# Kernel tuning notes

Hardware: AMD Instinct MI355X
Metric: run time of the kernel (lower is better)

The kernel has to match this reference:

```python
import jax, jax.numpy as jnp
import numpy as np

WINDOW_SIZE = 7
NB_HEADS = 8


def _relative_position_index(ws: int) -> np.ndarray:
    coords = np.stack(np.meshgrid(np.arange(ws), np.arange(ws), indexing='ij'))  # [2, ws, ws]
    flat = coords.reshape(2, -1)  # [2, ws*ws]
    rel = flat[:, :, None] - flat[:, None, :]  # [2, N, N]
    rel = rel.transpose(1, 2, 0)
    rel[:, :, 0] += ws - 1
    rel[:, :, 1] += ws - 1
    rel[:, :, 0] *= 2 * ws - 1
    return rel.sum(-1).astype(np.int64)  # [N, N]


def setup_inputs() -> dict:
    key = jax.random.key(0)
    ks = jax.random.split(key, 7)
    B_, N, C = 2048, WINDOW_SIZE * WINDOW_SIZE, 256
    nW = 64
    return {
        'x': jax.random.normal(ks[0], (B_, N, C), dtype=jnp.float32),
        'mask': jax.random.normal(ks[1], (nW, N, N), dtype=jnp.float32),
        'qkv_w': jax.random.normal(ks[2], (C, 3 * C), dtype=jnp.float32) * 0.02,
        'qkv_b': jax.random.normal(ks[3], (3 * C,), dtype=jnp.float32) * 0.02,
        'proj_w': jax.random.normal(ks[4], (C, C), dtype=jnp.float32) * 0.02,
        'proj_b': jax.random.normal(ks[5], (C,), dtype=jnp.float32) * 0.02,
        'bias_table': jax.random.normal(ks[6], ((2 * WINDOW_SIZE - 1) ** 2, NB_HEADS), dtype=jnp.float32) * 0.02,
    }


def reference(x, mask, qkv_w, qkv_b, proj_w, proj_b, bias_table):
    B_, N, C = x.shape
    h = NB_HEADS
    d = C // h
    rpi = jnp.asarray(_relative_position_index(WINDOW_SIZE))  # [N, N] int

    qkv = x @ qkv_w + qkv_b  # [B_, N, 3C]
    qkv = qkv.reshape(B_, N, 3, h, d).transpose(2, 0, 3, 1, 4)  # [3, B_, h, N, d]
    q, k, v = qkv[0], qkv[1], qkv[2]

    scale = d ** -0.5
    attn = jnp.einsum('bhnd,bhmd->bhnm', q * scale, k)  # [B_, h, N, N]

    # relative position bias gather: [N*N, h] -> [h, N, N]
    bias = bias_table[rpi.reshape(-1)].reshape(N, N, h).transpose(2, 0, 1)
    attn = attn + bias[None]

    nW = mask.shape[0]
    attn = attn.reshape(B_ // nW, nW, h, N, N) + mask[None, :, None]  # broadcast mask over heads
    attn = attn.reshape(B_, h, N, N)
    attn = jax.nn.softmax(attn, axis=-1)

    out = jnp.einsum('bhnm,bhmd->bhnd', attn, v)  # [B_, h, N, d]
    out = out.transpose(0, 2, 1, 3).reshape(B_, N, C)
    return out @ proj_w + proj_b
```

## Files before the change

### kernel.cpp

```cpp
#include <hip/hip_runtime.h>
#include <hip/hip_bf16.h>

typedef __attribute__((ext_vector_type(8))) short bf16x8;
typedef __attribute__((ext_vector_type(4))) float f32x4;

__device__ __forceinline__ void load_lds16(const void* g, void* l) {
    __builtin_amdgcn_global_load_lds(
        (const __attribute__((address_space(1))) unsigned int*)g,
        (__attribute__((address_space(3))) unsigned int*)l, 16, 0, 0);
}

__global__ void k_cvt_x(const float* __restrict__ x, __hip_bfloat16* __restrict__ xb, int n4) {
    for (int i = blockIdx.x * blockDim.x + threadIdx.x; i < n4; i += gridDim.x * blockDim.x) {
        float4 v = ((const float4*)x)[i];
        union { ushort4 u; __hip_bfloat16 h[4]; } o;
        o.h[0] = __float2bfloat16(v.x); o.h[1] = __float2bfloat16(v.y);
        o.h[2] = __float2bfloat16(v.z); o.h[3] = __float2bfloat16(v.w);
        ((ushort4*)xb)[i] = o.u;
    }
}

__global__ void k_prep(const float* __restrict__ qkv_w, const float* __restrict__ qkv_b,
                       const float* __restrict__ proj_w, const float* __restrict__ bias_table,
                       const float* __restrict__ mask,
                       __hip_bfloat16* __restrict__ qwT, __hip_bfloat16* __restrict__ pwT,
                       float* __restrict__ qb_s, float* __restrict__ cbt) {
    const float scale = 0.17677669529663687f;
    const int P1 = 768 * 256, P2 = P1 + 256 * 256, P3 = P2 + 768, P4 = P3 + 64 * 8 * 4 * 4 * 64;
    int i = blockIdx.x * 256 + threadIdx.x;
    if (i < P1) {
        int nc = i >> 8, kc = i & 255;
        float v = qkv_w[kc * 768 + nc];
        if (nc < 256) v *= scale;
        qwT[i] = __float2bfloat16(v);
    } else if (i < P2) {
        int j = i - P1;
        int nc = j >> 8, kc = j & 255;
        pwT[j] = __float2bfloat16(proj_w[kc * 256 + nc]);
    } else if (i < P3) {
        int j = i - P2;
        qb_s[j] = qkv_b[j] * (j < 256 ? scale : 1.f);
    } else if (i < P4) {
        int j = i - P3;
        int w = j >> 13;
        int h = (j >> 10) & 7;
        int rt = (j >> 8) & 3;
        int ct = (j >> 6) & 3;
        int lane = j & 63;
        int m = ct * 16 + (lane & 15);
        f32x4 v;
#pragma unroll
        for (int reg = 0; reg < 4; ++reg) {
            int n = rt * 16 + 4 * (lane >> 4) + reg;
            float val;
            if (m >= 49) val = -1e30f;
            else if (n >= 49) val = 0.f;
            else {
                int i1 = n / 7, j1 = n % 7, i2 = m / 7, j2 = m % 7;
                int rpi = (i1 - i2 + 6) * 13 + (j1 - j2 + 6);
                val = bias_table[rpi * 8 + h] + mask[(w * 49 + n) * 49 + m];
            }
            v[reg] = val;
        }
        ((f32x4*)cbt)[j] = v;
    }
}

template <bool OUT_BF16>
__global__ __launch_bounds__(256, 2)
void gemm_bt(const __hip_bfloat16* __restrict__ A,
             const __hip_bfloat16* __restrict__ BT,
             const float* __restrict__ bias,
             void* __restrict__ Cout,
             int M, int N, int K, int gridN) {
    __shared__ alignas(16) __hip_bfloat16 sA[2][128][64];
    __shared__ alignas(16) __hip_bfloat16 sB[2][128][64];
    const int nwg = gridDim.x, bid = blockIdx.x;
    const int qq = nwg >> 3, rr = nwg & 7;
    const int xc = bid & 7, oo = bid >> 3;
    const int wg = (xc < rr ? xc * (qq + 1) : rr * (qq + 1) + (xc - rr) * qq) + oo;
    const int bm = wg / gridN, bn = wg % gridN;

    const int tid = threadIdx.x, wid = tid >> 6, lane = tid & 63;
    const int g = lane >> 4, c0 = lane & 15;
    const int r8 = lane >> 3;
    const int sl = (lane & 7) ^ r8;
    const int wrow = (wid >> 1) * 64, wcol = (wid & 1) * 64;
    const __hip_bfloat16* Abase = A + (size_t)bm * 128 * K;
    const __hip_bfloat16* Bbase = BT + (size_t)bn * 128 * K;
    const int KT = K >> 6;

    f32x4 acc[4][4];
#pragma unroll
    for (int i = 0; i < 4; ++i)
#pragma unroll
        for (int j = 0; j < 4; ++j)
#pragma unroll
            for (int r = 0; r < 4; ++r) acc[i][j][r] = 0.f;

    auto stage = [&](int buf, int kt) {
        const __hip_bfloat16* Ak = Abase + kt * 64;
        const __hip_bfloat16* Bk = Bbase + kt * 64;
        char* la = (char*)&sA[buf][0][0];
        char* lb = (char*)&sB[buf][0][0];
#pragma unroll
        for (int i = 0; i < 4; ++i) {
            int chunk = wid * 4 + i;
            int row = chunk * 8 + r8;
            load_lds16(Ak + (size_t)row * K + sl * 8, la + chunk * 1024);
            load_lds16(Bk + (size_t)row * K + sl * 8, lb + chunk * 1024);
        }
    };

    stage(0, 0);
    __syncthreads();
    for (int kt = 0; kt < KT; ++kt) {
        int cur = kt & 1;
        if (kt + 1 < KT) stage(cur ^ 1, kt + 1);
        const char* la = (const char*)&sA[cur][0][0];
        const char* lb = (const char*)&sB[cur][0][0];
#pragma unroll
        for (int ks = 0; ks < 2; ++ks) {
            bf16x8 af[4], bfr[4];
            int sbyte = ((ks * 4 + g) ^ (c0 & 7)) * 16;
#pragma unroll
            for (int t = 0; t < 4; ++t) {
                int ra = wrow + t * 16 + c0;
                af[t] = *(const bf16x8*)(la + ra * 128 + sbyte);
                int rb = wcol + t * 16 + c0;
                bfr[t] = *(const bf16x8*)(lb + rb * 128 + sbyte);
            }
#pragma unroll
            for (int rt = 0; rt < 4; ++rt)
#pragma unroll
                for (int ct = 0; ct < 4; ++ct)
                    acc[rt][ct] = __builtin_amdgcn_mfma_f32_16x16x32_bf16(
                        af[rt], bfr[ct], acc[rt][ct], 0, 0, 0);
        }
        __syncthreads();
    }

    float bv[4];
#pragma unroll
    for (int ct = 0; ct < 4; ++ct) bv[ct] = bias[bn * 128 + wcol + ct * 16 + c0];
#pragma unroll
    for (int rt = 0; rt < 4; ++rt) {
#pragma unroll
        for (int ct = 0; ct < 4; ++ct) {
#pragma unroll
            for (int reg = 0; reg < 4; ++reg) {
                int row = bm * 128 + wrow + rt * 16 + g * 4 + reg;
                int col = bn * 128 + wcol + ct * 16 + c0;
                float v = acc[rt][ct][reg] + bv[ct];
                if (OUT_BF16)
                    ((__hip_bfloat16*)Cout)[(size_t)row * N + col] = __float2bfloat16(v);
                else
                    ((float*)Cout)[(size_t)row * N + col] = v;
            }
        }
    }
}

__global__ __launch_bounds__(64)
void attn_win(const __hip_bfloat16* __restrict__ qkv,
              const float* __restrict__ cbt,
              __hip_bfloat16* __restrict__ attout) {
    __shared__ alignas(16) __hip_bfloat16 vt[32][72];
    __shared__ alignas(16) __hip_bfloat16 pl[52][64];
    const int blk = blockIdx.x;
    const int w = blk >> 8, h = (blk >> 5) & 7, rep = blk & 31;
    const int b = rep * 64 + w;
    const int lane = threadIdx.x & 63, g = lane >> 4, c0 = lane & 15;
    const __hip_bfloat16* qb = qkv + (size_t)b * 49 * 768 + h * 32;
    const bf16x8 z8 = {};

    bf16x8 kf[4], qf[4];
#pragma unroll
    for (int ct = 0; ct < 4; ++ct) {
        int m = ct * 16 + c0;
        kf[ct] = (m < 49) ? *(const bf16x8*)(qb + (size_t)m * 768 + 256 + g * 8) : z8;
    }
#pragma unroll
    for (int rt = 0; rt < 4; ++rt) {
        int n = rt * 16 + c0;
        qf[rt] = (n < 49) ? *(const bf16x8*)(qb + (size_t)n * 768 + g * 8) : z8;
    }

#pragma unroll
    for (int it = 0; it < 4; ++it) {
        int q = it * 64 + lane;
        int m = q >> 2, c8 = (q & 3) * 8;
        if (m < 49) {
            bf16x8 v8 = *(const bf16x8*)(qb + (size_t)m * 768 + 512 + c8);
#pragma unroll
            for (int j = 0; j < 8; ++j)
                *(short*)&vt[c8 + j][m] = v8[j];
        }
    }
    for (int i = lane; i < 32 * 15; i += 64) {
        int c = i / 15, m = 49 + i % 15;
        vt[c][m] = __float2bfloat16(0.f);
    }

    const f32x4* cbb = (const f32x4*)cbt + ((size_t)(w * 8 + h)) * 1024;
    const f32x4 zf = {0.f, 0.f, 0.f, 0.f};

#pragma unroll
    for (int rt = 0; rt < 4; ++rt) {
        f32x4 cb[4];
#pragma unroll
        for (int ct = 0; ct < 4; ++ct) cb[ct] = cbb[(rt * 4 + ct) * 64 + lane];
        f32x4 s[4];
        __builtin_amdgcn_s_setprio(1);
#pragma unroll
        for (int ct = 0; ct < 4; ++ct)
            s[ct] = __builtin_amdgcn_mfma_f32_16x16x32_bf16(qf[rt], kf[ct], zf, 0, 0, 0);
        __builtin_amdgcn_s_setprio(0);
#pragma unroll
        for (int ct = 0; ct < 4; ++ct)
#pragma unroll
            for (int reg = 0; reg < 4; ++reg) s[ct][reg] += cb[ct][reg];
#pragma unroll
        for (int reg = 0; reg < 4; ++reg) {
            int n = rt * 16 + 4 * g + reg;
            float mx = fmaxf(fmaxf(s[0][reg], s[1][reg]), fmaxf(s[2][reg], s[3][reg]));
            mx = fmaxf(mx, __shfl_xor(mx, 1));
            mx = fmaxf(mx, __shfl_xor(mx, 2));
            mx = fmaxf(mx, __shfl_xor(mx, 4));
            mx = fmaxf(mx, __shfl_xor(mx, 8));
            float sum = 0.f;
#pragma unroll
            for (int ct = 0; ct < 4; ++ct) {
                float e = __expf(s[ct][reg] - mx);
                s[ct][reg] = e;
                sum += e;
            }
            sum += __shfl_xor(sum, 1);
            sum += __shfl_xor(sum, 2);
            sum += __shfl_xor(sum, 4);
            sum += __shfl_xor(sum, 8);
            float inv = 1.f / sum;
            if (n < 52) {
#pragma unroll
                for (int ct = 0; ct < 4; ++ct) {
                    int m = ct * 16 + c0;
                    int byte = (n * 128 + m * 2) ^ ((n & 7) << 4);
                    *(__hip_bfloat16*)((char*)&pl[0][0] + byte) = __float2bfloat16(s[ct][reg] * inv);
                }
            }
        }
    }
    __syncthreads();

    f32x4 o[4][2];
#pragma unroll
    for (int rt = 0; rt < 4; ++rt)
#pragma unroll
        for (int ci = 0; ci < 2; ++ci)
#pragma unroll
            for (int r = 0; r < 4; ++r) o[rt][ci][r] = 0.f;
#pragma unroll
    for (int kt = 0; kt < 2; ++kt) {
        bf16x8 pa[4], vb[2];
#pragma unroll
        for (int rt = 0; rt < 4; ++rt) {
            int row = rt * 16 + c0;
            int rc = row < 52 ? row : 51;
            int byte = rc * 128 + (((kt * 4 + g) ^ (rc & 7)) << 4);
            pa[rt] = *(const bf16x8*)((const char*)&pl[0][0] + byte);
        }
#pragma unroll
        for (int ci = 0; ci < 2; ++ci)
            vb[ci] = *(const bf16x8*)(&vt[ci * 16 + c0][kt * 32 + g * 8]);
        __builtin_amdgcn_s_setprio(1);
#pragma unroll
        for (int rt = 0; rt < 4; ++rt)
#pragma unroll
            for (int ci = 0; ci < 2; ++ci)
                o[rt][ci] = __builtin_amdgcn_mfma_f32_16x16x32_bf16(pa[rt], vb[ci], o[rt][ci], 0, 0, 0);
        __builtin_amdgcn_s_setprio(0);
    }
    __hip_bfloat16* ob = attout + (size_t)b * 49 * 256 + h * 32;
#pragma unroll
    for (int rt = 0; rt < 4; ++rt) {
#pragma unroll
        for (int reg = 0; reg < 4; ++reg) {
            int n = rt * 16 + 4 * g + reg;
            if (n < 49) {
#pragma unroll
                for (int ci = 0; ci < 2; ++ci)
                    ob[(size_t)n * 256 + ci * 16 + c0] = __float2bfloat16(o[rt][ci][reg]);
            }
        }
    }
}

extern "C" void kernel_launch(void* const* d_in, const int* in_sizes, int n_in,
                              void* d_out, int out_size, void* d_ws, size_t ws_size,
                              hipStream_t stream) {
    const float* x          = (const float*)d_in[0];
    const float* mask       = (const float*)d_in[1];
    const float* qkv_w      = (const float*)d_in[2];
    const float* qkv_b      = (const float*)d_in[3];
    const float* proj_w     = (const float*)d_in[4];
    const float* proj_b     = (const float*)d_in[5];
    const float* bias_table = (const float*)d_in[6];

    const int C = 256, N3 = 768, NN = 49;
    const int M  = in_sizes[0] / C;
    const int B_ = M / NN;

    char* ws = (char*)d_ws;
    __hip_bfloat16* qkv_ws = (__hip_bfloat16*)ws;
    size_t off = (size_t)M * N3 * 2;
    __hip_bfloat16* xb  = (__hip_bfloat16*)(ws + off);
    __hip_bfloat16* att = xb;
    off += (size_t)M * C * 2;
    __hip_bfloat16* qwT = (__hip_bfloat16*)(ws + off); off += (size_t)N3 * C * 2;
    __hip_bfloat16* pwT = (__hip_bfloat16*)(ws + off); off += (size_t)C * C * 2;
    float* qb_s = (float*)(ws + off); off += (size_t)N3 * 4;
    float* cbt  = (float*)(ws + off); off += (size_t)64 * 8 * 4096 * 4;

    int n4 = (int)((size_t)M * C / 4);
    k_cvt_x<<<2048, 256, 0, stream>>>(x, xb, n4);
    int prep_total = 768 * 256 + 256 * 256 + 768 + 64 * 8 * 4 * 4 * 64;
    k_prep<<<(prep_total + 255) / 256, 256, 0, stream>>>(qkv_w, qkv_b, proj_w, bias_table, mask,
                                                         qwT, pwT, qb_s, cbt);
    gemm_bt<true><<<(N3 / 128) * (M / 128), 256, 0, stream>>>(xb, qwT, qb_s, qkv_ws, M, N3, C, N3 / 128);
    attn_win<<<B_ * 8, 64, 0, stream>>>(qkv_ws, cbt, att);
    gemm_bt<false><<<(C / 128) * (M / 128), 256, 0, stream>>>(att, pwT, proj_b, d_out, M, C, C, C / 128);
}
```

Baseline: 362.7 us.

## Fuse x conversion, QKV GEMM, window attention and projection into one kernel

Replaces the separate x-to-bf16 conversion, tiled QKV GEMM, per-head attention kernel and projection GEMM with a single kernel that handles one window per 512-thread block, with one wave per head. The window's x, Q/K/V, softmax probabilities and attention output stay in LDS, so the bf16 copy of x and the qkv and attention intermediates are never written to or read back from HBM. In exchange, every block re-reads the full QKV and projection weight matrices from global memory (expected to be served mostly from L2) with no LDS staging. The roughly 148 KB of LDS per block also limits occupancy to very few waves per CU.

After: 371.4 us. 2.4% more time.

```diff
diff --git a/kernel.cpp b/kernel.cpp
--- a/kernel.cpp
+++ b/kernel.cpp
@@ -4,20 +4,9 @@
 typedef __attribute__((ext_vector_type(8))) short bf16x8;
 typedef __attribute__((ext_vector_type(4))) float f32x4;
 
-__device__ __forceinline__ void load_lds16(const void* g, void* l) {
-    __builtin_amdgcn_global_load_lds(
-        (const __attribute__((address_space(1))) unsigned int*)g,
-        (__attribute__((address_space(3))) unsigned int*)l, 16, 0, 0);
-}
-
-__global__ void k_cvt_x(const float* __restrict__ x, __hip_bfloat16* __restrict__ xb, int n4) {
-    for (int i = blockIdx.x * blockDim.x + threadIdx.x; i < n4; i += gridDim.x * blockDim.x) {
-        float4 v = ((const float4*)x)[i];
-        union { ushort4 u; __hip_bfloat16 h[4]; } o;
-        o.h[0] = __float2bfloat16(v.x); o.h[1] = __float2bfloat16(v.y);
-        o.h[2] = __float2bfloat16(v.z); o.h[3] = __float2bfloat16(v.w);
-        ((ushort4*)xb)[i] = o.u;
-    }
+static __device__ __forceinline__ short b16(float f) {
+    __hip_bfloat16 h = __float2bfloat16(f);
+    return *reinterpret_cast<short*>(&h);
 }
 
 __global__ void k_prep(const float* __restrict__ qkv_w, const float* __restrict__ qkv_b,
@@ -66,143 +55,104 @@
     }
 }
 
-template <bool OUT_BF16>
-__global__ __launch_bounds__(256, 2)
-void gemm_bt(const __hip_bfloat16* __restrict__ A,
-             const __hip_bfloat16* __restrict__ BT,
-             const float* __restrict__ bias,
-             void* __restrict__ Cout,
-             int M, int N, int K, int gridN) {
-    __shared__ alignas(16) __hip_bfloat16 sA[2][128][64];
-    __shared__ alignas(16) __hip_bfloat16 sB[2][128][64];
-    const int nwg = gridDim.x, bid = blockIdx.x;
-    const int qq = nwg >> 3, rr = nwg & 7;
-    const int xc = bid & 7, oo = bid >> 3;
-    const int wg = (xc < rr ? xc * (qq + 1) : rr * (qq + 1) + (xc - rr) * qq) + oo;
-    const int bm = wg / gridN, bn = wg % gridN;
-
-    const int tid = threadIdx.x, wid = tid >> 6, lane = tid & 63;
-    const int g = lane >> 4, c0 = lane & 15;
-    const int r8 = lane >> 3;
-    const int sl = (lane & 7) ^ r8;
-    const int wrow = (wid >> 1) * 64, wcol = (wid & 1) * 64;
-    const __hip_bfloat16* Abase = A + (size_t)bm * 128 * K;
-    const __hip_bfloat16* Bbase = BT + (size_t)bn * 128 * K;
-    const int KT = K >> 6;
-
-    f32x4 acc[4][4];
-#pragma unroll
-    for (int i = 0; i < 4; ++i)
-#pragma unroll
-        for (int j = 0; j < 4; ++j)
-#pragma unroll
-            for (int r = 0; r < 4; ++r) acc[i][j][r] = 0.f;
-
-    auto stage = [&](int buf, int kt) {
-        const __hip_bfloat16* Ak = Abase + kt * 64;
-        const __hip_bfloat16* Bk = Bbase + kt * 64;
-        char* la = (char*)&sA[buf][0][0];
-        char* lb = (char*)&sB[buf][0][0];
-#pragma unroll
-        for (int i = 0; i < 4; ++i) {
-            int chunk = wid * 4 + i;
-            int row = chunk * 8 + r8;
-            load_lds16(Ak + (size_t)row * K + sl * 8, la + chunk * 1024);
-            load_lds16(Bk + (size_t)row * K + sl * 8, lb + chunk * 1024);
-        }
-    };
-
-    stage(0, 0);
+#define XS_OFF    0
+#define PL_OFF(h) ((h) * 6272)
+#define QK_OFF    50176
+#define QS(h)     (QK_OFF + (h) * 8000)
+#define KS(h)     (QK_OFF + (h) * 8000 + 4000)
+#define AS_OFF    QK_OFF
+#define VT(h)     (114176 + (h) * 4608)
+#define LDS_TOTAL 151040
+
+__global__ __launch_bounds__(512, 2)
+void win_fused(const float* __restrict__ x,
+               const __hip_bfloat16* __restrict__ qwT,
+               const __hip_bfloat16* __restrict__ pwT,
+               const float* __restrict__ qb_s,
+               const float* __restrict__ proj_b,
+               const float* __restrict__ cbt,
+               float* __restrict__ out) {
+    __shared__ alignas(16) char lds[LDS_TOTAL];
+    const int b = blockIdx.x;
+    const int tid = threadIdx.x;
+    const int h = tid >> 6, lane = tid & 63, g = lane >> 4, c0 = lane & 15;
+
+    const float* xw = x + (size_t)b * 12544;
+    for (int i = tid; i < 3136; i += 512) {
+        int row = i >> 6, col4 = i & 63;
+        float4 v = *(const float4*)(xw + row * 256 + col4 * 4);
+        union { unsigned long long u; short s[4]; } o;
+        o.s[0] = b16(v.x); o.s[1] = b16(v.y); o.s[2] = b16(v.z); o.s[3] = b16(v.w);
+        int byte = row * 512 + (((col4 >> 1) ^ (row & 7)) << 4) + (col4 & 1) * 8;
+        *(unsigned long long*)(lds + byte) = o.u;
+    }
     __syncthreads();
-    for (int kt = 0; kt < KT; ++kt) {
-        int cur = kt & 1;
-        if (kt + 1 < KT) stage(cur ^ 1, kt + 1);
-        const char* la = (const char*)&sA[cur][0][0];
-        const char* lb = (const char*)&sB[cur][0][0];
-#pragma unroll
-        for (int ks = 0; ks < 2; ++ks) {
-            bf16x8 af[4], bfr[4];
-            int sbyte = ((ks * 4 + g) ^ (c0 & 7)) * 16;
-#pragma unroll
-            for (int t = 0; t < 4; ++t) {
-                int ra = wrow + t * 16 + c0;
-                af[t] = *(const bf16x8*)(la + ra * 128 + sbyte);
-                int rb = wcol + t * 16 + c0;
-                bfr[t] = *(const bf16x8*)(lb + rb * 128 + sbyte);
-            }
-#pragma unroll
-            for (int rt = 0; rt < 4; ++rt)
-#pragma unroll
-                for (int ct = 0; ct < 4; ++ct)
-                    acc[rt][ct] = __builtin_amdgcn_mfma_f32_16x16x32_bf16(
-                        af[rt], bfr[ct], acc[rt][ct], 0, 0, 0);
-        }
-        __syncthreads();
-    }
-
-    float bv[4];
-#pragma unroll
-    for (int ct = 0; ct < 4; ++ct) bv[ct] = bias[bn * 128 + wcol + ct * 16 + c0];
-#pragma unroll
-    for (int rt = 0; rt < 4; ++rt) {
-#pragma unroll
-        for (int ct = 0; ct < 4; ++ct) {
-#pragma unroll
-            for (int reg = 0; reg < 4; ++reg) {
-                int row = bm * 128 + wrow + rt * 16 + g * 4 + reg;
-                int col = bn * 128 + wcol + ct * 16 + c0;
-                float v = acc[rt][ct][reg] + bv[ct];
-                if (OUT_BF16)
-                    ((__hip_bfloat16*)Cout)[(size_t)row * N + col] = __float2bfloat16(v);
-                else
-                    ((float*)Cout)[(size_t)row * N + col] = v;
-            }
-        }
-    }
-}
-
-__global__ __launch_bounds__(64)
-void attn_win(const __hip_bfloat16* __restrict__ qkv,
-              const float* __restrict__ cbt,
-              __hip_bfloat16* __restrict__ attout) {
-    __shared__ alignas(16) __hip_bfloat16 vt[32][72];
-    __shared__ alignas(16) __hip_bfloat16 pl[52][64];
-    const int blk = blockIdx.x;
-    const int w = blk >> 8, h = (blk >> 5) & 7, rep = blk & 31;
-    const int b = rep * 64 + w;
-    const int lane = threadIdx.x & 63, g = lane >> 4, c0 = lane & 15;
-    const __hip_bfloat16* qb = qkv + (size_t)b * 49 * 768 + h * 32;
-    const bf16x8 z8 = {};
-
-    bf16x8 kf[4], qf[4];
-#pragma unroll
-    for (int ct = 0; ct < 4; ++ct) {
-        int m = ct * 16 + c0;
-        kf[ct] = (m < 49) ? *(const bf16x8*)(qb + (size_t)m * 768 + 256 + g * 8) : z8;
-    }
-#pragma unroll
-    for (int rt = 0; rt < 4; ++rt) {
-        int n = rt * 16 + c0;
-        qf[rt] = (n < 49) ? *(const bf16x8*)(qb + (size_t)n * 768 + g * 8) : z8;
-    }
-
-#pragma unroll
-    for (int it = 0; it < 4; ++it) {
-        int q = it * 64 + lane;
-        int m = q >> 2, c8 = (q & 3) * 8;
-        if (m < 49) {
-            bf16x8 v8 = *(const bf16x8*)(qb + (size_t)m * 768 + 512 + c8);
-#pragma unroll
-            for (int j = 0; j < 8; ++j)
-                *(short*)&vt[c8 + j][m] = v8[j];
-        }
-    }
-    for (int i = lane; i < 32 * 15; i += 64) {
-        int c = i / 15, m = 49 + i % 15;
-        vt[c][m] = __float2bfloat16(0.f);
-    }
-
-    const f32x4* cbb = (const f32x4*)cbt + ((size_t)(w * 8 + h)) * 1024;
+
+    f32x4 acc[3][4][2];
+#pragma unroll
+    for (int q3 = 0; q3 < 3; ++q3)
+#pragma unroll
+        for (int rt = 0; rt < 4; ++rt)
+#pragma unroll
+            for (int ct2 = 0; ct2 < 2; ++ct2)
+#pragma unroll
+                for (int r = 0; r < 4; ++r) acc[q3][rt][ct2][r] = 0.f;
+
+#pragma unroll
+    for (int kt = 0; kt < 8; ++kt) {
+        bf16x8 af[4];
+#pragma unroll
+        for (int rt = 0; rt < 4; ++rt) {
+            int row = rt * 16 + c0;
+            af[rt] = *(const bf16x8*)(lds + row * 512 + (((kt * 4 + g) ^ (c0 & 7)) << 4));
+        }
+#pragma unroll
+        for (int q3 = 0; q3 < 3; ++q3) {
+#pragma unroll
+            for (int ct2 = 0; ct2 < 2; ++ct2) {
+                bf16x8 bw = *(const bf16x8*)(qwT + (size_t)(q3 * 256 + h * 32 + ct2 * 16 + c0) * 256
+                                             + kt * 32 + g * 8);
+#pragma unroll
+                for (int rt = 0; rt < 4; ++rt)
+                    acc[q3][rt][ct2] = __builtin_amdgcn_mfma_f32_16x16x32_bf16(
+                        af[rt], bw, acc[q3][rt][ct2], 0, 0, 0);
+            }
+        }
+    }
+#pragma unroll
+    for (int q3 = 0; q3 < 3; ++q3) {
+#pragma unroll
+        for (int ct2 = 0; ct2 < 2; ++ct2) {
+            float bias = qb_s[q3 * 256 + h * 32 + ct2 * 16 + c0];
+            int d0 = ct2 * 16 + c0;
+#pragma unroll
+            for (int rt = 0; rt < 4; ++rt) {
+#pragma unroll
+                for (int reg = 0; reg < 4; ++reg) {
+                    int n = rt * 16 + 4 * g + reg;
+                    if (q3 == 2) {
+                        short sv = (n < 49) ? b16(acc[q3][rt][ct2][reg] + bias) : (short)0;
+                        *(short*)(lds + VT(h) + d0 * 144 + n * 2) = sv;
+                    } else if (n < 49) {
+                        short sv = b16(acc[q3][rt][ct2][reg] + bias);
+                        if (q3 == 0) *(short*)(lds + QS(h) + n * 80 + d0 * 2) = sv;
+                        else         *(short*)(lds + KS(h) + n * 80 + d0 * 2) = sv;
+                    }
+                }
+            }
+        }
+    }
+    __syncthreads();
+
+    bf16x8 qf[4], kf[4];
+#pragma unroll
+    for (int t = 0; t < 4; ++t) {
+        int n = t * 16 + c0;
+        int nc = n < 49 ? n : 48;
+        qf[t] = *(const bf16x8*)(lds + QS(h) + nc * 80 + g * 16);
+        kf[t] = *(const bf16x8*)(lds + KS(h) + nc * 80 + g * 16);
+    }
+    const f32x4* cbb = (const f32x4*)cbt + ((size_t)((b & 63) * 8 + h)) * 1024;
     const f32x4 zf = {0.f, 0.f, 0.f, 0.f};
 
 #pragma unroll
@@ -240,12 +190,12 @@
             sum += __shfl_xor(sum, 4);
             sum += __shfl_xor(sum, 8);
             float inv = 1.f / sum;
-            if (n < 52) {
+            if (n < 49) {
 #pragma unroll
                 for (int ct = 0; ct < 4; ++ct) {
                     int m = ct * 16 + c0;
                     int byte = (n * 128 + m * 2) ^ ((n & 7) << 4);
-                    *(__hip_bfloat16*)((char*)&pl[0][0] + byte) = __float2bfloat16(s[ct][reg] * inv);
+                    *(short*)(lds + PL_OFF(h) + byte) = b16(s[ct][reg] * inv);
                 }
             }
         }
@@ -260,18 +210,18 @@
 #pragma unroll
             for (int r = 0; r < 4; ++r) o[rt][ci][r] = 0.f;
 #pragma unroll
-    for (int kt = 0; kt < 2; ++kt) {
+    for (int kt2 = 0; kt2 < 2; ++kt2) {
         bf16x8 pa[4], vb[2];
 #pragma unroll
         for (int rt = 0; rt < 4; ++rt) {
             int row = rt * 16 + c0;
-            int rc = row < 52 ? row : 51;
-            int byte = rc * 128 + (((kt * 4 + g) ^ (rc & 7)) << 4);
-            pa[rt] = *(const bf16x8*)((const char*)&pl[0][0] + byte);
+            int rc = row < 49 ? row : 48;
+            int byte = rc * 128 + (((kt2 * 4 + g) ^ (rc & 7)) << 4);
+            pa[rt] = *(const bf16x8*)(lds + PL_OFF(h) + byte);
         }
 #pragma unroll
         for (int ci = 0; ci < 2; ++ci)
-            vb[ci] = *(const bf16x8*)(&vt[ci * 16 + c0][kt * 32 + g * 8]);
+            vb[ci] = *(const bf16x8*)(lds + VT(h) + (ci * 16 + c0) * 144 + (kt2 * 32 + g * 8) * 2);
         __builtin_amdgcn_s_setprio(1);
 #pragma unroll
         for (int rt = 0; rt < 4; ++rt)
@@ -280,16 +230,61 @@
                 o[rt][ci] = __builtin_amdgcn_mfma_f32_16x16x32_bf16(pa[rt], vb[ci], o[rt][ci], 0, 0, 0);
         __builtin_amdgcn_s_setprio(0);
     }
-    __hip_bfloat16* ob = attout + (size_t)b * 49 * 256 + h * 32;
 #pragma unroll
     for (int rt = 0; rt < 4; ++rt) {
 #pragma unroll
-        for (int reg = 0; reg < 4; ++reg) {
-            int n = rt * 16 + 4 * g + reg;
-            if (n < 49) {
-#pragma unroll
-                for (int ci = 0; ci < 2; ++ci)
-                    ob[(size_t)n * 256 + ci * 16 + c0] = __float2bfloat16(o[rt][ci][reg]);
+        for (int ci = 0; ci < 2; ++ci) {
+#pragma unroll
+            for (int reg = 0; reg < 4; ++reg) {
+                int n = rt * 16 + 4 * g + reg;
+                if (n < 49) {
+                    int col = h * 32 + ci * 16 + c0;
+                    *(short*)(lds + AS_OFF + n * 512 + (((col >> 3) ^ (n & 7)) << 4) + (col & 7) * 2)
+                        = b16(o[rt][ci][reg]);
+                }
+            }
+        }
+    }
+    __syncthreads();
+
+    f32x4 po[4][2];
+#pragma unroll
+    for (int rt = 0; rt < 4; ++rt)
+#pragma unroll
+        for (int ct2 = 0; ct2 < 2; ++ct2)
+#pragma unroll
+            for (int r = 0; r < 4; ++r) po[rt][ct2][r] = 0.f;
+#pragma unroll
+    for (int kt = 0; kt < 8; ++kt) {
+        bf16x8 paf[4], pb[2];
+#pragma unroll
+        for (int rt = 0; rt < 4; ++rt) {
+            int row = rt * 16 + c0;
+            paf[rt] = *(const bf16x8*)(lds + AS_OFF + row * 512 + (((kt * 4 + g) ^ (c0 & 7)) << 4));
+        }
+#pragma unroll
+        for (int ct2 = 0; ct2 < 2; ++ct2)
+            pb[ct2] = *(const bf16x8*)(pwT + (size_t)(h * 32 + ct2 * 16 + c0) * 256 + kt * 32 + g * 8);
+#pragma unroll
+        for (int rt = 0; rt < 4; ++rt)
+#pragma unroll
+            for (int ct2 = 0; ct2 < 2; ++ct2)
+                po[rt][ct2] = __builtin_amdgcn_mfma_f32_16x16x32_bf16(
+                    paf[rt], pb[ct2], po[rt][ct2], 0, 0, 0);
+    }
+    float* ob = out + (size_t)b * 12544;
+    float pbias[2];
+#pragma unroll
+    for (int ct2 = 0; ct2 < 2; ++ct2) pbias[ct2] = proj_b[h * 32 + ct2 * 16 + c0];
+#pragma unroll
+    for (int rt = 0; rt < 4; ++rt) {
+#pragma unroll
+        for (int ct2 = 0; ct2 < 2; ++ct2) {
+#pragma unroll
+            for (int reg = 0; reg < 4; ++reg) {
+                int n = rt * 16 + 4 * g + reg;
+                if (n < 49)
+                    ob[(size_t)n * 256 + h * 32 + ct2 * 16 + c0] = po[rt][ct2][reg] + pbias[ct2];
             }
         }
     }
@@ -306,27 +301,19 @@
     const float* proj_b     = (const float*)d_in[5];
     const float* bias_table = (const float*)d_in[6];
 
-    const int C = 256, N3 = 768, NN = 49;
+    const int C = 256, NN = 49;
     const int M  = in_sizes[0] / C;
     const int B_ = M / NN;
 
     char* ws = (char*)d_ws;
-    __hip_bfloat16* qkv_ws = (__hip_bfloat16*)ws;
-    size_t off = (size_t)M * N3 * 2;
-    __hip_bfloat16* xb  = (__hip_bfloat16*)(ws + off);
-    __hip_bfloat16* att = xb;
-    off += (size_t)M * C * 2;
-    __hip_bfloat16* qwT = (__hip_bfloat16*)(ws + off); off += (size_t)N3 * C * 2;
-    __hip_bfloat16* pwT = (__hip_bfloat16*)(ws + off); off += (size_t)C * C * 2;
-    float* qb_s = (float*)(ws + off); off += (size_t)N3 * 4;
+    __hip_bfloat16* qwT = (__hip_bfloat16*)ws;
+    size_t off = (size_t)768 * 256 * 2;
+    __hip_bfloat16* pwT = (__hip_bfloat16*)(ws + off); off += (size_t)256 * 256 * 2;
+    float* qb_s = (float*)(ws + off); off += (size_t)768 * 4;
     float* cbt  = (float*)(ws + off); off += (size_t)64 * 8 * 4096 * 4;
 
-    int n4 = (int)((size_t)M * C / 4);
-    k_cvt_x<<<2048, 256, 0, stream>>>(x, xb, n4);
     int prep_total = 768 * 256 + 256 * 256 + 768 + 64 * 8 * 4 * 4 * 64;
     k_prep<<<(prep_total + 255) / 256, 256, 0, stream>>>(qkv_w, qkv_b, proj_w, bias_table, mask,
                                                          qwT, pwT, qb_s, cbt);
-    gemm_bt<true><<<(N3 / 128) * (M / 128), 256, 0, stream>>>(xb, qwT, qb_s, qkv_ws, M, N3, C, N3 / 128);
-    attn_win<<<B_ * 8, 64, 0, stream>>>(qkv_ws, cbt, att);
-    gemm_bt<false><<<(C / 128) * (M / 128), 256, 0, stream>>>(att, pwT, proj_b, d_out, M, C, C, C / 128);
+    win_fused<<<B_, 512, 0, stream>>>(x, qwT, pwT, qb_s, proj_b, cbt, (float*)d_out);
 }
```
